# Performance work log

Measured on AMD Instinct MI355X. Metric: run time of the kernel, lower is better.

The kernel has to match this reference:

```python
import jax, jax.numpy as jnp
import numpy as np

N_NODES = 50000
N_EDGES = 1200000
N_REL = 45
IN_C, HID_C, OUT_C = 64, 32, 16


def setup_inputs() -> dict:
    key = jax.random.key(0)
    ks = jax.random.split(key, 9)
    x = jax.random.normal(ks[0], (N_NODES, IN_C), dtype=jnp.float32)
    edge_index = jax.random.randint(ks[1], (2, N_EDGES), 0, N_NODES, dtype=jnp.int64)
    edge_type = jax.random.randint(ks[2], (N_EDGES,), 0, N_REL, dtype=jnp.int64)
    s = 0.05
    W1 = jax.random.normal(ks[3], (N_REL, IN_C, HID_C), dtype=jnp.float32) * s
    root1 = jax.random.normal(ks[4], (IN_C, HID_C), dtype=jnp.float32) * s
    b1 = jax.random.normal(ks[5], (HID_C,), dtype=jnp.float32) * s
    W2 = jax.random.normal(ks[6], (N_REL, HID_C, OUT_C), dtype=jnp.float32) * s
    root2 = jax.random.normal(ks[7], (HID_C, OUT_C), dtype=jnp.float32) * s
    b2 = jax.random.normal(ks[8], (OUT_C,), dtype=jnp.float32) * s
    return {"x": x, "edge_index": edge_index, "edge_type": edge_type,
            "W1": W1, "root1": root1, "b1": b1,
            "W2": W2, "root2": root2, "b2": b2}


def rgcn_conv(x, edge_index, edge_type, W, root, b):
    # PyG RGCNConv: out_i = x_i @ root + b + sum_r mean_{j in N_r(i)} (x_j @ W_r)
    N = x.shape[0]
    R = W.shape[0]
    src, dst = edge_index[0], edge_index[1]
    # per-relation transform of all nodes: [R, N, out]
    h = jnp.einsum('ni,rio->rno', x, W)
    # per-edge message: gather transformed src feature for edge's relation
    msg = h[edge_type, src]                      # [E, out]
    # segment id combines (relation, dst) for per-relation mean aggregation
    seg = edge_type * N + dst                    # [E]
    sums = jax.ops.segment_sum(msg, seg, num_segments=R * N)        # [R*N, out]
    cnt = jax.ops.segment_sum(jnp.ones((msg.shape[0],), x.dtype), seg,
                              num_segments=R * N)                   # [R*N]
    mean = sums / jnp.maximum(cnt, 1.0)[:, None]
    agg = mean.reshape(R, N, -1).sum(axis=0)     # sum over relations -> [N, out]
    return agg + x @ root + b


def reference(x, edge_index, edge_type, W1, root1, b1, W2, root2, b2):
    h = rgcn_conv(x, edge_index, edge_type, W1, root1, b1)
    h = jax.nn.relu(h)
    out = rgcn_conv(h, edge_index, edge_type, W2, root2, b2)
    return out
```

## Files before the change

kernel.cpp:

```cpp
#include <hip/hip_runtime.h>
#include <hip/hip_fp16.h>
#include <cstdint>
#include <cstddef>

#define NN   50000
#define NE   1200000
#define NR   45
#define INC  64
#define HIDC 32
#define OUTC 16
#define MAXE 1202880
#define NCHUNK (MAXE/64)
#define EPB 4096
#define NB  ((NE + EPB - 1) / EPB)
#define QDW 6250
#define QDD 12500
#define NTILE ((NN + 255) / 256)


typedef _Float16 f16x8 __attribute__((ext_vector_type(8)));
typedef float    f32x4 __attribute__((ext_vector_type(4)));

union F16Bits { unsigned short u; _Float16 f; };
union ABFrag   { uint4 u; f16x8 f; };

__global__ __launch_bounds__(256) void preph_k(const float* __restrict__ W1,
                                               const float* __restrict__ W2,
                                               const float* __restrict__ x,
                                               const int* __restrict__ ei,
                                               const int* __restrict__ et,
                                               __half* __restrict__ W1f,
                                               __half* __restrict__ W2f,
                                               __half* __restrict__ xh,
                                               unsigned* __restrict__ ghist,
                                               unsigned* __restrict__ rsorted,
                                               unsigned* __restrict__ flagbuf) {
    __shared__ unsigned lh[4 * 48];
    int t = threadIdx.x, b = blockIdx.x;
    int wv = t >> 6;
    if (t < 192) lh[t] = 0;
    __syncthreads();
    if (b < NB) {
        #pragma unroll
        for (int it = 0; it < EPB / 256; ++it) {
            int e = b * EPB + it * 256 + t;
            if (e < NE) {
                int r = et[e], src = ei[e], dst = ei[NE + e];
                if ((unsigned)r < NR && (unsigned)src < NN && (unsigned)dst < NN)
                    atomicAdd(&lh[wv * 48 + r], 1u);
            }
        }
    }
    __syncthreads();
    if (b < NB && t < NR)
        ghist[t * NB + b] = lh[t] + lh[48 + t] + lh[96 + t] + lh[144 + t];
    int g = b * 256 + t;
    int gthreads = gridDim.x * 256;
    for (int i = g; i < MAXE; i += gthreads) rsorted[i] = 0xFFFFFFFFu;
    if (b == 0) flagbuf[t] = 0;
    if (g < NR * 2048) {
        int r = g >> 11, rem = g & 2047;
        int kb = rem >> 10, nb = (rem >> 9) & 1;
        int lane = (rem >> 3) & 63, j = rem & 7;
        int k = kb * 32 + (lane >> 4) * 8 + j;
        int n = nb * 16 + (lane & 15);
        W1f[g] = __float2half(W1[(r * INC + k) * HIDC + n]);
    }
    if (g < NR * 512) {
        int r = g >> 9, rem = g & 511;
        int lane = (rem >> 3) & 63, j = rem & 7;
        int k = (lane >> 4) * 8 + j;
        int kc = (k >> 1) + ((k & 1) << 4);
        int n = lane & 15;
        W2f[g] = __float2half(W2[(r * HIDC + kc) * OUTC + n]);
    }
    if (g < NN * INC / 2) {
        float2 f = ((const float2*)x)[g];
        union { __half2 h; unsigned u; } cv;
        cv.h = __floats2half2_rn(f.x, f.y);
        ((unsigned*)xh)[g] = cv.u;
    }
}

__global__ __launch_bounds__(1024) void scat_k(const int* __restrict__ ei,
                                               const int* __restrict__ et,
                                               const unsigned* __restrict__ ghist,
                                               unsigned* __restrict__ rngs,
                                               int* __restrict__ chunkrel,
                                               unsigned* __restrict__ rsorted) {
    __shared__ unsigned reltot[NR];
    __shared__ unsigned mypart[NR];
    __shared__ unsigned relbase[NR + 1];
    __shared__ unsigned lbase[NR], lcur[NR];
    int t = threadIdx.x, bx = blockIdx.x;
    if (t < NR) {
        unsigned total = 0, part = 0;
        const unsigned* __restrict__ row = ghist + t * NB;
        for (int b = 0; b < NB; ++b) {
            if (b == bx) part = total;
            total += row[b];
        }
        reltot[t] = total;
        mypart[t] = part;
        lcur[t] = 0;
    }
    __syncthreads();
    if (t == 0) {
        unsigned acc = 0;
        for (int r = 0; r < NR; ++r) {
            relbase[r] = acc;
            acc += ((reltot[r] + 63u) >> 6) << 6;
        }
        relbase[NR] = acc;
    }
    __syncthreads();
    if (t < NR) lbase[t] = relbase[t] + mypart[t];
    __syncthreads();
    #pragma unroll
    for (int it = 0; it < EPB / 1024; ++it) {
        int e = bx * EPB + it * 1024 + t;
        if (e < NE) {
            int r = et[e], src = ei[e], dst = ei[NE + e];
            if ((unsigned)r < NR && (unsigned)src < NN && (unsigned)dst < NN) {
                unsigned local = atomicAdd(&lcur[r], 1u);
                rsorted[lbase[r] + local] = (unsigned)src | ((unsigned)dst << 16);
            }
        }
    }
    if (bx == 0) {
        if (t < NR) {
            rngs[2 * t]     = relbase[t];
            rngs[2 * t + 1] = relbase[t] + reltot[t];
        }
        for (int c = t; c < NCHUNK; c += 1024) {
            unsigned pos = (unsigned)c << 6;
            int lo = 0, hi = NR - 1;
            while (lo < hi) {
                int mid = (lo + hi + 1) >> 1;
                if (relbase[mid] <= pos) lo = mid; else hi = mid - 1;
            }
            chunkrel[c] = lo;
        }
    }
}

__global__ __launch_bounds__(1024) void relcnt_k(const unsigned* __restrict__ rsorted,
                                                 const unsigned* __restrict__ rngs,
                                                 unsigned short* __restrict__ cnt16,
                                                 unsigned short* __restrict__ rank16) {
    __shared__ unsigned lds[QDW];
    int r = blockIdx.x >> 2, q = blockIdx.x & 3, t = threadIdx.x;
    unsigned base = rngs[2 * r], end = rngs[2 * r + 1];
    unsigned dlo = q * QDD, dhi = dlo + QDD;
    for (int w = t; w < QDW; w += 1024) lds[w] = 0;
    __syncthreads();
    for (unsigned s = base + t; s < end; s += 1024) {
        unsigned d = rsorted[s] >> 16;
        if (d >= dlo && d < dhi) {
            unsigned off = d - dlo;
            unsigned old = atomicAdd(&lds[off >> 1], (off & 1) ? 0x10000u : 1u);
            rank16[s] = (unsigned short)((off & 1) ? (old >> 16) : (old & 0xFFFFu));
        }
    }
    __syncthreads();
    unsigned* __restrict__ cp = (unsigned*)(cnt16 + (size_t)r * NN + dlo);
    for (int w = t; w < QDW; w += 1024) cp[w] = lds[w];
}

__global__ __launch_bounds__(256) void dp_k(const unsigned short* __restrict__ cnt16,
                                            unsigned* __restrict__ packed,
                                            unsigned* __restrict__ rowptr,
                                            unsigned* __restrict__ flags) {
    __shared__ unsigned wsum[4];
    __shared__ unsigned excl_s;
    int t = threadIdx.x, b = blockIdx.x;
    int lane = t & 63, wv = t >> 6;
    int dst = b * 256 + t;
    unsigned deg = 0;
    if (dst < NN) {
        unsigned run = 0;
        #pragma unroll 5
        for (int r = 0; r < NR; ++r) {
            unsigned c = cnt16[(size_t)r * NN + dst];
            F16Bits fb; fb.f = (_Float16)(c ? 1.0f / (float)c : 0.0f);
            packed[(size_t)r * NN + dst] = (run & 0xFFFFu) | ((unsigned)fb.u << 16);
            run += c;
        }
        deg = run;
    }
    unsigned s = deg;
    #pragma unroll
    for (int off = 1; off < 64; off <<= 1) {
        unsigned n = __shfl_up(s, off);
        if (lane >= off) s += n;
    }
    if (lane == 63) wsum[wv] = s;
    __syncthreads();
    unsigned waveoff = 0;
    if (wv > 0) waveoff += wsum[0];
    if (wv > 1) waveoff += wsum[1];
    if (wv > 2) waveoff += wsum[2];
    unsigned blockT = wsum[0] + wsum[1] + wsum[2] + wsum[3];
    unsigned local_excl = waveoff + s - deg;
    if (t == 0) {
        if (b == 0) {
            excl_s = 0;
            atomicExch(&flags[0], 0x80000000u | blockT);
        } else {
            atomicExch(&flags[b], 0x40000000u | blockT);
            unsigned ex = 0;
            int p = b - 1;
            while (p >= 0) {
                unsigned f = atomicAdd(&flags[p], 0u);
                unsigned st = f >> 30;
                if (st == 0) continue;
                ex += f & 0x3FFFFFFFu;
                if (st >= 2) break;
                --p;
            }
            excl_s = ex;
            atomicExch(&flags[b], 0x80000000u | (ex + blockT));
        }
    }
    __syncthreads();
    unsigned ex = excl_s;
    if (dst < NN) rowptr[dst] = ex + local_excl;
    if (b == (int)gridDim.x - 1 && t == 0) rowptr[NN] = ex + blockT;
}

__global__ __launch_bounds__(256) void finalize_k(const unsigned* __restrict__ rsorted,
                                                  const unsigned short* __restrict__ rank16,
                                                  const unsigned* __restrict__ packed,
                                                  const unsigned* __restrict__ rowptr,
                                                  const int* __restrict__ chunkrel,
                                                  uint2* __restrict__ pedges) {
    int s = blockIdx.x * 256 + threadIdx.x;
    if (s >= MAXE) return;
    unsigned v = rsorted[s];
    unsigned dst = v >> 16;
    if (dst >= NN) { pedges[s] = make_uint2(0u, 0x80000000u); return; }
    int r = chunkrel[s >> 6];
    unsigned pk = packed[(size_t)r * NN + dst];
    unsigned dpos = rowptr[dst] + (pk & 0xFFFFu) + (unsigned)rank16[s];
    pedges[s] = make_uint2((v & 0xFFFFu) | (pk & 0xFFFF0000u),
                           dpos | ((unsigned)r << 25));
}

__global__ __launch_bounds__(256) void msg1_k(const __half* __restrict__ xh,
                                              const __half* __restrict__ W1f,
                                              const uint2* __restrict__ pedges,
                                              __half* __restrict__ msg) {
    int tid = threadIdx.x;
    int lane = tid & 63;
    int wave = (blockIdx.x * 256 + tid) >> 6;
    if (wave >= NCHUNK) return;
    int e = (wave << 6) + lane;
    uint2 er = pedges[e];
    int w1 = (int)er.y;
    int rel = __builtin_amdgcn_readfirstlane((w1 >> 25) & 63);
    F16Bits fb; fb.u = (unsigned short)(er.x >> 16);
    float sc = (float)fb.f;
    int src = er.x & 0xFFFF;
    int drow = (w1 < 0) ? NE : (w1 & 0x1FFFFFF);
    const uint4* __restrict__ wf = (const uint4*)W1f + (size_t)rel * 256;
    ABFrag b00, b01, b10, b11;
    b00.u = wf[0 * 64 + lane];
    b01.u = wf[1 * 64 + lane];
    b10.u = wf[2 * 64 + lane];
    b11.u = wf[3 * 64 + lane];
    int quad = lane >> 4, col = lane & 15;
    ABFrag a0[4], a1[4];
    #pragma unroll
    for (int tl = 0; tl < 4; ++tl) {
        int s = __shfl(src, tl * 16 + col);
        const uint4* __restrict__ xp = (const uint4*)(xh + (size_t)s * INC) + quad;
        a0[tl].u = xp[0];
        a1[tl].u = xp[4];
    }
    #pragma unroll
    for (int tl = 0; tl < 4; ++tl) {
        f32x4 acc0 = {0.f, 0.f, 0.f, 0.f}, acc1 = {0.f, 0.f, 0.f, 0.f};
        acc0 = __builtin_amdgcn_mfma_f32_16x16x32_f16(a0[tl].f, b00.f, acc0, 0, 0, 0);
        acc0 = __builtin_amdgcn_mfma_f32_16x16x32_f16(a1[tl].f, b10.f, acc0, 0, 0, 0);
        acc1 = __builtin_amdgcn_mfma_f32_16x16x32_f16(a0[tl].f, b01.f, acc1, 0, 0, 0);
        acc1 = __builtin_amdgcn_mfma_f32_16x16x32_f16(a1[tl].f, b11.f, acc1, 0, 0, 0);
        #pragma unroll
        for (int i = 0; i < 4; ++i) {
            int ee = tl * 16 + quad * 4 + i;
            int dr   = __shfl(drow, ee);
            float si = __shfl(sc, ee);
            union { __half2 h; unsigned u; } cv;
            cv.h = __floats2half2_rn(acc0[i] * si, acc1[i] * si);
            ((unsigned*)(msg + (size_t)dr * HIDC))[col] = cv.u;
        }
    }
}

__global__ __launch_bounds__(256) void msg2_k(const __half* __restrict__ hh,
                                              const __half* __restrict__ W2f,
                                              const uint2* __restrict__ pedges,
                                              __half* __restrict__ msg) {
    int tid = threadIdx.x;
    int lane = tid & 63;
    int wave = (blockIdx.x * 256 + tid) >> 6;
    if (wave >= NCHUNK) return;
    int e = (wave << 6) + lane;
    uint2 er = pedges[e];
    int w1 = (int)er.y;
    int rel = __builtin_amdgcn_readfirstlane((w1 >> 25) & 63);
    F16Bits fb; fb.u = (unsigned short)(er.x >> 16);
    float sc = (float)fb.f;
    int src = er.x & 0xFFFF;
    int drow = (w1 < 0) ? NE : (w1 & 0x1FFFFFF);
    ABFrag bf;
    bf.u = ((const uint4*)W2f + (size_t)rel * 64)[lane];
    int quad = lane >> 4, col = lane & 15;
    ABFrag a[4];
    #pragma unroll
    for (int tl = 0; tl < 4; ++tl) {
        int s = __shfl(src, tl * 16 + col);
        a[tl].u = *((const uint4*)(hh + (size_t)s * HIDC) + quad);
    }
    #pragma unroll
    for (int tl = 0; tl < 4; ++tl) {
        f32x4 acc = {0.f, 0.f, 0.f, 0.f};
        acc = __builtin_amdgcn_mfma_f32_16x16x32_f16(a[tl].f, bf.f, acc, 0, 0, 0);
        #pragma unroll
        for (int i = 0; i < 4; ++i) {
            int ee = tl * 16 + quad * 4 + i;
            int dr   = __shfl(drow, ee);
            float si = __shfl(sc, ee);
            float v  = acc[i] * si;
            float p  = __shfl_xor(v, 8);
            if (col < 8) {
                union { __half2 h; unsigned u; } cv;
                cv.h = __floats2half2_rn(v, p);
                ((unsigned*)(msg + (size_t)dr * OUTC))[col] = cv.u;
            }
        }
    }
}

__global__ __launch_bounds__(256) void gather1_k(const __half* __restrict__ xh,
                                                 const float* __restrict__ root1,
                                                 const float* __restrict__ b1,
                                                 const __half* __restrict__ msg,
                                                 const unsigned* __restrict__ rowptr,
                                                 __half* __restrict__ hh) {
    __shared__ float sr[INC * HIDC];
    for (int k = threadIdx.x; k < INC * HIDC; k += 256) sr[k] = root1[k];
    __syncthreads();
    int wid = (blockIdx.x * 256 + threadIdx.x) >> 6;
    int lane = threadIdx.x & 63;
    int c2 = lane & 15, sub = lane >> 4;
    unsigned k0 = rowptr[wid], k1 = rowptr[wid + 1];
    float accx = 0.f, accy = 0.f;
    for (unsigned k = k0 + sub; k < k1; k += 4) {
        union { __half2 hh2; unsigned u; } cv;
        cv.u = ((const unsigned*)(msg + (size_t)k * HIDC))[c2];
        float2 f = __half22float2(cv.hh2);
        accx += f.x; accy += f.y;
    }
    const uint4* __restrict__ xp =
        (const uint4*)(xh + (size_t)wid * INC + sub * 16);
    union { uint4 u; __half2 h[4]; } ua, ub;
    ua.u = xp[0];
    ub.u = xp[1];
    #pragma unroll
    for (int q = 0; q < 4; ++q) {
        float2 f = __half22float2(ua.h[q]);
        int in = sub * 16 + 2 * q;
        accx = fmaf(f.x, sr[in * HIDC + c2], accx);
        accy = fmaf(f.x, sr[in * HIDC + c2 + 16], accy);
        accx = fmaf(f.y, sr[(in + 1) * HIDC + c2], accx);
        accy = fmaf(f.y, sr[(in + 1) * HIDC + c2 + 16], accy);
    }
    #pragma unroll
    for (int q = 0; q < 4; ++q) {
        float2 f = __half22float2(ub.h[q]);
        int in = sub * 16 + 8 + 2 * q;
        accx = fmaf(f.x, sr[in * HIDC + c2], accx);
        accy = fmaf(f.x, sr[in * HIDC + c2 + 16], accy);
        accx = fmaf(f.y, sr[(in + 1) * HIDC + c2], accx);
        accy = fmaf(f.y, sr[(in + 1) * HIDC + c2 + 16], accy);
    }
    accx += __shfl_xor(accx, 16); accy += __shfl_xor(accy, 16);
    accx += __shfl_xor(accx, 32); accy += __shfl_xor(accy, 32);
    if (sub == 0) {
        float vx = accx + b1[c2], vy = accy + b1[c2 + 16];
        union { __half2 h2; unsigned u; } cv;
        cv.h2 = __floats2half2_rn(vx > 0.f ? vx : 0.f, vy > 0.f ? vy : 0.f);
        ((unsigned*)hh)[(size_t)wid * (HIDC / 2) + c2] = cv.u;
    }
}

__global__ __launch_bounds__(256) void gather2_k(const __half* __restrict__ hh,
                                                 const float* __restrict__ root2,
                                                 const float* __restrict__ b2,
                                                 const __half* __restrict__ msg,
                                                 const unsigned* __restrict__ rowptr,
                                                 float* __restrict__ out) {
    __shared__ float sr[HIDC * OUTC];
    for (int k = threadIdx.x; k < HIDC * OUTC; k += 256) sr[k] = root2[k];
    __syncthreads();
    int wid = (blockIdx.x * 256 + threadIdx.x) >> 6;
    int lane = threadIdx.x & 63;
    int c2 = lane & 7, sub = lane >> 3;
    unsigned k0 = rowptr[wid], k1 = rowptr[wid + 1];
    float accx = 0.f, accy = 0.f;
    for (unsigned k = k0 + sub; k < k1; k += 8) {
        union { __half2 hh2; unsigned u; } cv;
        cv.u = ((const unsigned*)(msg + (size_t)k * OUTC))[c2];
        float2 f = __half22float2(cv.hh2);
        accx += f.x; accy += f.y;
    }
    uint2 hw = *(const uint2*)(hh + (size_t)wid * HIDC + sub * 4);
    union { __half2 h2; unsigned u; } ca, cb;
    ca.u = hw.x; cb.u = hw.y;
    float2 ha = __half22float2(ca.h2), hb = __half22float2(cb.h2);
    float hs[4] = { ha.x, ha.y, hb.x, hb.y };
    #pragma unroll
    for (int j = 0; j < 4; ++j) {
        int in = 2 * sub + (j >> 1) + ((j & 1) << 4);
        accx = fmaf(hs[j], sr[in * OUTC + c2], accx);
        accy = fmaf(hs[j], sr[in * OUTC + c2 + 8], accy);
    }
    accx += __shfl_xor(accx, 8);  accy += __shfl_xor(accy, 8);
    accx += __shfl_xor(accx, 16); accy += __shfl_xor(accy, 16);
    accx += __shfl_xor(accx, 32); accy += __shfl_xor(accy, 32);
    if (sub == 0) {
        out[(size_t)wid * OUTC + c2]     = accx + b2[c2];
        out[(size_t)wid * OUTC + c2 + 8] = accy + b2[c2 + 8];
    }
}

extern "C" void kernel_launch(void* const* d_in, const int* in_sizes, int n_in,
                              void* d_out, int out_size, void* d_ws, size_t ws_size,
                              hipStream_t stream) {
    const float* x     = (const float*)d_in[0];
    const int*   ei    = (const int*)d_in[1];
    const int*   et    = (const int*)d_in[2];
    const float* W1    = (const float*)d_in[3];
    const float* root1 = (const float*)d_in[4];
    const float* b1    = (const float*)d_in[5];
    const float* W2    = (const float*)d_in[6];
    const float* root2 = (const float*)d_in[7];
    const float* b2    = (const float*)d_in[8];
    float* out = (float*)d_out;

    char* ws = (char*)d_ws;
    size_t o = 0;
    auto alloc = [&](size_t bytes) -> char* {
        char* p = ws + o;
        o = (o + bytes + 255) & ~(size_t)255;
        return p;
    };
    unsigned* rsorted = (unsigned*)alloc((size_t)MAXE * 4);
    unsigned* flagbuf = (unsigned*)alloc(256 * 4);
    unsigned* ghist   = (unsigned*)alloc((size_t)NR * NB * 4);
    unsigned* rngs    = (unsigned*)alloc((size_t)NR * 2 * 4);
    int*      chunkrel= (int*)     alloc((size_t)NCHUNK * 4);
    unsigned short* rank16 = (unsigned short*)alloc((size_t)MAXE * 2);
    unsigned short* cnt16  = (unsigned short*)alloc((size_t)NR * NN * 2);
    unsigned* packed  = (unsigned*)alloc((size_t)NR * NN * 4);
    unsigned* rowptr  = (unsigned*)alloc(((size_t)NN + 1) * 4);
    uint2*    pedges  = (uint2*)   alloc((size_t)MAXE * 8);
    __half*   W1f     = (__half*)  alloc((size_t)NR * 2048 * 2);
    __half*   W2f     = (__half*)  alloc((size_t)NR * 512 * 2);
    __half*   xh      = (__half*)  alloc((size_t)NN * INC * 2);
    __half*   hh      = (__half*)  alloc((size_t)NN * HIDC * 2);
    char*     msgraw  = alloc(((size_t)NE + 1) * 64);
    __half*   msg1    = (__half*)msgraw;
    __half*   msg2    = (__half*)msgraw;

    int prep_grid = NN * INC / 2 / 256;
    preph_k   <<<prep_grid, 256, 0, stream>>>(W1, W2, x, ei, et, W1f, W2f, xh,
                                              ghist, rsorted, flagbuf);
    scat_k    <<<NB, 1024, 0, stream>>>(ei, et, ghist, rngs, chunkrel, rsorted);
    relcnt_k  <<<4 * NR, 1024, 0, stream>>>(rsorted, rngs, cnt16, rank16);
    dp_k      <<<NTILE, 256, 0, stream>>>(cnt16, packed, rowptr, flagbuf + 32);
    finalize_k<<<(MAXE + 255) / 256, 256, 0, stream>>>(rsorted, rank16, packed,
                                                       rowptr, chunkrel, pedges);
    msg1_k    <<<(MAXE + 255) / 256, 256, 0, stream>>>(xh, W1f, pedges, msg1);
    gather1_k <<<NN * 64 / 256, 256, 0, stream>>>(xh, root1, b1, msg1, rowptr, hh);
    msg2_k    <<<(MAXE + 255) / 256, 256, 0, stream>>>(hh, W2f, pedges, msg2);
    gather2_k <<<NN * 64 / 256, 256, 0, stream>>>(hh, root2, b2, msg2, rowptr, out);
}
```

Measured before the change: 310.7 us.

## Vectorize gather kernels with 16-byte message loads and register-held root weights

Both gather kernels are restructured so each lane loads a 16-byte chunk of a message row, processing more edges per wave in parallel, instead of 4-byte chunks. The root weight matrices and bias are repacked into interleaved float2 layouts in the prep kernel, so each lane keeps its slice in registers and the shared-memory staging and block barrier go away. This trades more accumulators and a longer shuffle reduction for fewer, wider memory transactions and vectorized output stores.

```diff
diff --git a/kernel.cpp b/kernel.cpp
--- a/kernel.cpp
+++ b/kernel.cpp
@@ -29,9 +29,15 @@
                                                const float* __restrict__ x,
                                                const int* __restrict__ ei,
                                                const int* __restrict__ et,
+                                               const float* __restrict__ root1,
+                                               const float* __restrict__ root2,
+                                               const float* __restrict__ b1,
                                                __half* __restrict__ W1f,
                                                __half* __restrict__ W2f,
                                                __half* __restrict__ xh,
+                                               float2* __restrict__ rootp1,
+                                               float2* __restrict__ rootp2,
+                                               float2* __restrict__ b1p,
                                                unsigned* __restrict__ ghist,
                                                unsigned* __restrict__ rsorted,
                                                unsigned* __restrict__ flagbuf) {
@@ -80,6 +86,15 @@
         cv.h = __floats2half2_rn(f.x, f.y);
         ((unsigned*)xh)[g] = cv.u;
     }
+    if (g < 1024) {
+        int in = g >> 4, w = g & 15;
+        rootp1[g] = make_float2(root1[in * HIDC + w], root1[in * HIDC + w + 16]);
+    }
+    if (g < 256) {
+        int in = g >> 3, w = g & 7;
+        rootp2[g] = make_float2(root2[in * OUTC + w], root2[in * OUTC + w + 8]);
+    }
+    if (g < 16) b1p[g] = make_float2(b1[g], b1[g + 16]);
 }
 
 __global__ __launch_bounds__(1024) void scat_k(const int* __restrict__ ei,
@@ -342,95 +357,122 @@
 }
 
 __global__ __launch_bounds__(256) void gather1_k(const __half* __restrict__ xh,
-                                                 const float* __restrict__ root1,
-                                                 const float* __restrict__ b1,
+                                                 const float2* __restrict__ rootp1,
+                                                 const float2* __restrict__ b1p,
                                                  const __half* __restrict__ msg,
                                                  const unsigned* __restrict__ rowptr,
                                                  __half* __restrict__ hh) {
-    __shared__ float sr[INC * HIDC];
-    for (int k = threadIdx.x; k < INC * HIDC; k += 256) sr[k] = root1[k];
-    __syncthreads();
-    int wid = (blockIdx.x * 256 + threadIdx.x) >> 6;
-    int lane = threadIdx.x & 63;
-    int c2 = lane & 15, sub = lane >> 4;
+    int tid = threadIdx.x;
+    int lane = tid & 63;
+    int wid = (blockIdx.x * 256 + tid) >> 6;
+    int g = lane >> 2, j = lane & 3;
     unsigned k0 = rowptr[wid], k1 = rowptr[wid + 1];
-    float accx = 0.f, accy = 0.f;
-    for (unsigned k = k0 + sub; k < k1; k += 4) {
-        union { __half2 hh2; unsigned u; } cv;
-        cv.u = ((const unsigned*)(msg + (size_t)k * HIDC))[c2];
-        float2 f = __half22float2(cv.hh2);
-        accx += f.x; accy += f.y;
-    }
-    const uint4* __restrict__ xp =
-        (const uint4*)(xh + (size_t)wid * INC + sub * 16);
-    union { uint4 u; __half2 h[4]; } ua, ub;
-    ua.u = xp[0];
-    ub.u = xp[1];
-    #pragma unroll
-    for (int q = 0; q < 4; ++q) {
-        float2 f = __half22float2(ua.h[q]);
-        int in = sub * 16 + 2 * q;
-        accx = fmaf(f.x, sr[in * HIDC + c2], accx);
-        accy = fmaf(f.x, sr[in * HIDC + c2 + 16], accy);
-        accx = fmaf(f.y, sr[(in + 1) * HIDC + c2], accx);
-        accy = fmaf(f.y, sr[(in + 1) * HIDC + c2 + 16], accy);
-    }
-    #pragma unroll
-    for (int q = 0; q < 4; ++q) {
-        float2 f = __half22float2(ub.h[q]);
-        int in = sub * 16 + 8 + 2 * q;
-        accx = fmaf(f.x, sr[in * HIDC + c2], accx);
-        accy = fmaf(f.x, sr[in * HIDC + c2 + 16], accy);
-        accx = fmaf(f.y, sr[(in + 1) * HIDC + c2], accx);
-        accy = fmaf(f.y, sr[(in + 1) * HIDC + c2 + 16], accy);
-    }
-    accx += __shfl_xor(accx, 16); accy += __shfl_xor(accy, 16);
-    accx += __shfl_xor(accx, 32); accy += __shfl_xor(accy, 32);
-    if (sub == 0) {
-        float vx = accx + b1[c2], vy = accy + b1[c2 + 16];
-        union { __half2 h2; unsigned u; } cv;
-        cv.h2 = __floats2half2_rn(vx > 0.f ? vx : 0.f, vy > 0.f ? vy : 0.f);
-        ((unsigned*)hh)[(size_t)wid * (HIDC / 2) + c2] = cv.u;
+    float2 rw[4][4];
+    #pragma unroll
+    for (int i = 0; i < 4; ++i) {
+        const float4* __restrict__ rp =
+            (const float4*)rootp1 + ((4 * g + i) << 3) + 2 * j;
+        float4 u0 = rp[0], u1 = rp[1];
+        rw[i][0] = make_float2(u0.x, u0.y);
+        rw[i][1] = make_float2(u0.z, u0.w);
+        rw[i][2] = make_float2(u1.x, u1.y);
+        rw[i][3] = make_float2(u1.z, u1.w);
+    }
+    float acc[8] = {0.f, 0.f, 0.f, 0.f, 0.f, 0.f, 0.f, 0.f};
+    for (unsigned k = k0 + g; k < k1; k += 16) {
+        uint4 v = ((const uint4*)(msg + (size_t)k * HIDC))[j];
+        union { unsigned u; __half2 h; } c0, c1, c2, c3;
+        c0.u = v.x; c1.u = v.y; c2.u = v.z; c3.u = v.w;
+        float2 f0 = __half22float2(c0.h), f1 = __half22float2(c1.h);
+        float2 f2 = __half22float2(c2.h), f3 = __half22float2(c3.h);
+        acc[0] += f0.x; acc[1] += f0.y;
+        acc[2] += f1.x; acc[3] += f1.y;
+        acc[4] += f2.x; acc[5] += f2.y;
+        acc[6] += f3.x; acc[7] += f3.y;
+    }
+    union { uint2 u; __half2 h[2]; } xv;
+    xv.u = ((const uint2*)(xh + (size_t)wid * INC))[g];
+    float2 xa = __half22float2(xv.h[0]), xb = __half22float2(xv.h[1]);
+    float xs[4] = { xa.x, xa.y, xb.x, xb.y };
+    #pragma unroll
+    for (int i = 0; i < 4; ++i) {
+        #pragma unroll
+        for (int q = 0; q < 4; ++q) {
+            acc[2 * q]     = fmaf(xs[i], rw[i][q].x, acc[2 * q]);
+            acc[2 * q + 1] = fmaf(xs[i], rw[i][q].y, acc[2 * q + 1]);
+        }
+    }
+    #pragma unroll
+    for (int off = 4; off < 64; off <<= 1) {
+        #pragma unroll
+        for (int q = 0; q < 8; ++q) acc[q] += __shfl_xor(acc[q], off);
+    }
+    if (g == 0) {
+        const float4* __restrict__ bp4 = (const float4*)b1p;
+        float4 bb0 = bp4[2 * j], bb1 = bp4[2 * j + 1];
+        float2 bq[4] = { make_float2(bb0.x, bb0.y), make_float2(bb0.z, bb0.w),
+                         make_float2(bb1.x, bb1.y), make_float2(bb1.z, bb1.w) };
+        unsigned um[4];
+        #pragma unroll
+        for (int q = 0; q < 4; ++q) {
+            float vx = acc[2 * q] + bq[q].x, vy = acc[2 * q + 1] + bq[q].y;
+            union { __half2 h2; unsigned u; } cv;
+            cv.h2 = __floats2half2_rn(vx > 0.f ? vx : 0.f, vy > 0.f ? vy : 0.f);
+            um[q] = cv.u;
+        }
+        ((uint4*)(hh + (size_t)wid * HIDC))[j] = make_uint4(um[0], um[1], um[2], um[3]);
     }
 }
 
 __global__ __launch_bounds__(256) void gather2_k(const __half* __restrict__ hh,
-                                                 const float* __restrict__ root2,
+                                                 const float2* __restrict__ rootp2,
                                                  const float* __restrict__ b2,
                                                  const __half* __restrict__ msg,
                                                  const unsigned* __restrict__ rowptr,
                                                  float* __restrict__ out) {
-    __shared__ float sr[HIDC * OUTC];
-    for (int k = threadIdx.x; k < HIDC * OUTC; k += 256) sr[k] = root2[k];
-    __syncthreads();
-    int wid = (blockIdx.x * 256 + threadIdx.x) >> 6;
-    int lane = threadIdx.x & 63;
-    int c2 = lane & 7, sub = lane >> 3;
+    int tid = threadIdx.x;
+    int lane = tid & 63;
+    int wid = (blockIdx.x * 256 + tid) >> 6;
+    int g = lane >> 1, j = lane & 1;
     unsigned k0 = rowptr[wid], k1 = rowptr[wid + 1];
-    float accx = 0.f, accy = 0.f;
-    for (unsigned k = k0 + sub; k < k1; k += 8) {
-        union { __half2 hh2; unsigned u; } cv;
-        cv.u = ((const unsigned*)(msg + (size_t)k * OUTC))[c2];
-        float2 f = __half22float2(cv.hh2);
-        accx += f.x; accy += f.y;
-    }
-    uint2 hw = *(const uint2*)(hh + (size_t)wid * HIDC + sub * 4);
-    union { __half2 h2; unsigned u; } ca, cb;
-    ca.u = hw.x; cb.u = hw.y;
-    float2 ha = __half22float2(ca.h2), hb = __half22float2(cb.h2);
-    float hs[4] = { ha.x, ha.y, hb.x, hb.y };
-    #pragma unroll
-    for (int j = 0; j < 4; ++j) {
-        int in = 2 * sub + (j >> 1) + ((j & 1) << 4);
-        accx = fmaf(hs[j], sr[in * OUTC + c2], accx);
-        accy = fmaf(hs[j], sr[in * OUTC + c2 + 8], accy);
-    }
-    accx += __shfl_xor(accx, 8);  accy += __shfl_xor(accy, 8);
-    accx += __shfl_xor(accx, 16); accy += __shfl_xor(accy, 16);
-    accx += __shfl_xor(accx, 32); accy += __shfl_xor(accy, 32);
-    if (sub == 0) {
-        out[(size_t)wid * OUTC + c2]     = accx + b2[c2];
-        out[(size_t)wid * OUTC + c2 + 8] = accy + b2[c2 + 8];
+    const float4* __restrict__ rp = (const float4*)rootp2 + (g << 2) + 2 * j;
+    float4 u0 = rp[0], u1 = rp[1];
+    float2 rw[4] = { make_float2(u0.x, u0.y), make_float2(u0.z, u0.w),
+                     make_float2(u1.x, u1.y), make_float2(u1.z, u1.w) };
+    float acc[8] = {0.f, 0.f, 0.f, 0.f, 0.f, 0.f, 0.f, 0.f};
+    for (unsigned k = k0 + g; k < k1; k += 32) {
+        uint4 v = ((const uint4*)(msg + (size_t)k * OUTC))[j];
+        union { unsigned u; __half2 h; } c0, c1, c2, c3;
+        c0.u = v.x; c1.u = v.y; c2.u = v.z; c3.u = v.w;
+        float2 f0 = __half22float2(c0.h), f1 = __half22float2(c1.h);
+        float2 f2 = __half22float2(c2.h), f3 = __half22float2(c3.h);
+        acc[0] += f0.x; acc[1] += f0.y;
+        acc[2] += f1.x; acc[3] += f1.y;
+        acc[4] += f2.x; acc[5] += f2.y;
+        acc[6] += f3.x; acc[7] += f3.y;
+    }
+    unsigned hw = ((const unsigned*)(hh + (size_t)wid * HIDC))[g & 15];
+    union { unsigned u; __half2 h; } hc; hc.u = hw;
+    float2 hf = __half22float2(hc.h);
+    float hv = (g < 16) ? hf.x : hf.y;
+    #pragma unroll
+    for (int q = 0; q < 4; ++q) {
+        acc[2 * q]     = fmaf(hv, rw[q].x, acc[2 * q]);
+        acc[2 * q + 1] = fmaf(hv, rw[q].y, acc[2 * q + 1]);
+    }
+    #pragma unroll
+    for (int off = 2; off < 64; off <<= 1) {
+        #pragma unroll
+        for (int q = 0; q < 8; ++q) acc[q] += __shfl_xor(acc[q], off);
+    }
+    if (g == 0) {
+        float* __restrict__ orow = out + (size_t)wid * OUTC;
+        float4 ba = ((const float4*)b2)[j];
+        float4 bb = ((const float4*)b2)[j + 2];
+        ((float4*)orow)[j] = make_float4(acc[0] + ba.x, acc[2] + ba.y,
+                                         acc[4] + ba.z, acc[6] + ba.w);
+        ((float4*)orow)[j + 2] = make_float4(acc[1] + bb.x, acc[3] + bb.y,
+                                             acc[5] + bb.z, acc[7] + bb.w);
     }
 }
 
@@ -469,12 +511,16 @@
     __half*   W2f     = (__half*)  alloc((size_t)NR * 512 * 2);
     __half*   xh      = (__half*)  alloc((size_t)NN * INC * 2);
     __half*   hh      = (__half*)  alloc((size_t)NN * HIDC * 2);
+    float2*   rootp1  = (float2*)  alloc(1024 * 8);
+    float2*   rootp2  = (float2*)  alloc(256 * 8);
+    float2*   b1p     = (float2*)  alloc(16 * 8);
     char*     msgraw  = alloc(((size_t)NE + 1) * 64);
     __half*   msg1    = (__half*)msgraw;
     __half*   msg2    = (__half*)msgraw;
 
     int prep_grid = NN * INC / 2 / 256;
-    preph_k   <<<prep_grid, 256, 0, stream>>>(W1, W2, x, ei, et, W1f, W2f, xh,
+    preph_k   <<<prep_grid, 256, 0, stream>>>(W1, W2, x, ei, et, root1, root2, b1,
+                                              W1f, W2f, xh, rootp1, rootp2, b1p,
                                               ghist, rsorted, flagbuf);
     scat_k    <<<NB, 1024, 0, stream>>>(ei, et, ghist, rngs, chunkrel, rsorted);
     relcnt_k  <<<4 * NR, 1024, 0, stream>>>(rsorted, rngs, cnt16, rank16);
@@ -482,7 +528,7 @@
     finalize_k<<<(MAXE + 255) / 256, 256, 0, stream>>>(rsorted, rank16, packed,
                                                        rowptr, chunkrel, pedges);
     msg1_k    <<<(MAXE + 255) / 256, 256, 0, stream>>>(xh, W1f, pedges, msg1);
-    gather1_k <<<NN * 64 / 256, 256, 0, stream>>>(xh, root1, b1, msg1, rowptr, hh);
+    gather1_k <<<NN * 64 / 256, 256, 0, stream>>>(xh, rootp1, b1p, msg1, rowptr, hh);
     msg2_k    <<<(MAXE + 255) / 256, 256, 0, stream>>>(hh, W2f, pedges, msg2);
-    gather2_k <<<NN * 64 / 256, 256, 0, stream>>>(hh, root2, b2, msg2, rowptr, out);
-}
+    gather2_k <<<NN * 64 / 256, 256, 0, stream>>>(hh, rootp2, b2, msg2, rowptr, out);
+}
```

After: 294.0 us. 1.06x faster.
